# Performance work log

Measured on AMD Instinct MI355X. Metric: run time of the kernel, lower is better.

Reference implementation:

```python
import jax, jax.numpy as jnp
import numpy as np

T, B, D, H = 512, 64, 256, 512


def setup_inputs() -> dict:
    key = jax.random.key(0)
    k1, k2, k3, k4 = jax.random.split(key, 4)
    x = jax.random.normal(k1, (T, B, D), dtype=jnp.float32)
    should_reset = jax.random.randint(k2, (T, B), 0, 2, dtype=jnp.int32)
    # Linear([x, h]) -> 4H gates, Haiku/PyTorch-style fan-in init scale
    scale = 1.0 / np.sqrt(D + H)
    W = jax.random.normal(k3, (D + H, 4 * H), dtype=jnp.float32) * scale
    b = jax.random.normal(k4, (4 * H,), dtype=jnp.float32) * scale
    return {"x": x, "should_reset": should_reset, "W": W, "b": b}


def reference(x, should_reset, W, b):
    """ResetLSTM forward (reverse=False). x:[T,B,D], should_reset:[T,B] -> [T,B,H]."""
    h0 = jnp.zeros((x.shape[1], H), dtype=x.dtype)
    c0 = jnp.zeros((x.shape[1], H), dtype=x.dtype)
    reset = should_reset.astype(x.dtype)[..., None]  # [T,B,1]

    def step(carry, inp):
        h, c = carry
        xt, rt = inp
        keep = 1.0 - rt
        h = h * keep
        c = c * keep
        gates = jnp.concatenate([xt, h], axis=-1) @ W + b  # [B,4H]
        i, g, f, o = jnp.split(gates, 4, axis=-1)
        f = jax.nn.sigmoid(f + 1.0)  # Haiku forget bias +1
        i = jax.nn.sigmoid(i)
        g = jnp.tanh(g)
        o = jax.nn.sigmoid(o)
        new_c = f * c + i * g
        new_h = o * jnp.tanh(new_c)
        return (new_h, new_c), new_h

    _, outputs = jax.lax.scan(step, (h0, c0), (x, reset))
    return outputs  # [T,B,H]
```

## Files before the change

### kernel.cpp

```cpp
#include <hip/hip_runtime.h>

#define TSTEPS 512
#define BATCH  64
#define DIN    256
#define HID    512
#define NCH    8
#define VR     512
#define NRB    16
#define NUB    32
#define NWG    512
#define NTHR   256
#define HSST   264
#define GST    67

typedef __attribute__((ext_vector_type(8))) _Float16 f16x8;
typedef __attribute__((ext_vector_type(4))) _Float16 f16x4;
typedef __attribute__((ext_vector_type(4))) float f32x4;
typedef __attribute__((ext_vector_type(2))) float f32x2;

#define MFMA16(A,B,C) __builtin_amdgcn_mfma_f32_16x16x32_f16(A,B,C,0,0,0)
#define ALDU64(p) __hip_atomic_load(const_cast<unsigned long long*>(p), __ATOMIC_RELAXED, __HIP_MEMORY_SCOPE_AGENT)
#define ALDU32(p) __hip_atomic_load(const_cast<unsigned*>(p), __ATOMIC_RELAXED, __HIP_MEMORY_SCOPE_AGENT)
#define ASTU32(p,v) __hip_atomic_store((p), (v), __ATOMIC_RELAXED, __HIP_MEMORY_SCOPE_AGENT)

__device__ __forceinline__ float sigm(float x) { return 1.0f / (1.0f + __expf(-x)); }

__global__ void conv_x(const float* __restrict__ x, _Float16* __restrict__ xh, int n4) {
  int i = blockIdx.x * 256 + threadIdx.x;
  if (i >= n4) return;
  float4 v = reinterpret_cast<const float4*>(x)[i];
  f16x4 o;
  o[0] = (_Float16)v.x; o[1] = (_Float16)v.y; o[2] = (_Float16)v.z; o[3] = (_Float16)v.w;
  *reinterpret_cast<f16x4*>(xh + (size_t)i * 4) = o;
}

__global__ void w_prep(const float* __restrict__ W,
                       _Float16* __restrict__ WxT, _Float16* __restrict__ WhT) {
  int idx = blockIdx.x * 256 + threadIdx.x;
  if (idx < NUB * 64 * 256) {
    int k = idx & 255, cc = (idx >> 8) & 63, ub = idx >> 14;
    int unit = cc >> 2, g = cc & 3;
    int gcol = g * HID + ub * 16 + unit;
    WxT[idx] = (_Float16)W[k * 2048 + gcol];
  } else if (idx < NUB * 64 * 256 + NUB * 64 * 512) {
    int j = idx - NUB * 64 * 256;
    int k = j & 511, cc = (j >> 9) & 63, ub = j >> 15;
    int unit = cc >> 2, g = cc & 3;
    int gcol = g * HID + ub * 16 + unit;
    WhT[j] = (_Float16)W[(DIN + k) * 2048 + gcol];
  }
}

__global__ void seg_prep(const int* __restrict__ rst, int* __restrict__ tS,
                         int* __restrict__ segLen, int* __restrict__ maxLenB) {
  __shared__ int sMax[NRB];
  const int b = threadIdx.x;
  if (b < NRB) sMax[b] = 0;
  __syncthreads();
  int cut[NCH + 1];
  cut[0] = 0; cut[NCH] = TSTEPS;
  for (int c = 1; c < NCH; ++c) {
    int t = c * 64;
    while (t < TSTEPS && rst[t * BATCH + b] == 0) ++t;
    cut[c] = t;
  }
  for (int c = 1; c < NCH; ++c) if (cut[c] < cut[c - 1]) cut[c] = cut[c - 1];
  for (int c = 0; c < NCH; ++c) {
    int vr = c * 64 + b;
    tS[vr] = cut[c];
    int L = cut[c + 1] - cut[c];
    segLen[vr] = L;
    atomicMax(&sMax[c * 2 + (b >> 5)], L);
  }
  __syncthreads();
  if (b < NRB) maxLenB[b] = sMax[b];
}

__global__ void __launch_bounds__(NTHR, 2)
lstm_persistent(const _Float16* __restrict__ xh,
                const int* __restrict__ rst,
                const float* __restrict__ bias,
                float* __restrict__ out,
                unsigned long long* __restrict__ hb,
                unsigned* __restrict__ flags,
                const _Float16* __restrict__ WxT,
                const _Float16* __restrict__ WhT,
                const int* __restrict__ tS,
                const int* __restrict__ segLen,
                const int* __restrict__ maxLenB) {
  __shared__ _Float16 hS[32 * HSST];
  __shared__ float gateS[32 * GST];
  __shared__ float biasS[64];

  const int tid = threadIdx.x, wg = blockIdx.x;
  const int rb = wg >> 5, ub = wg & 31;
  const int vr0 = rb * 32;
  const int lane = tid & 63, wave = tid >> 6;
  const int colA = lane & 15, klo = (lane >> 4) * 8;

  f16x8 wx[8], wh[16];
  {
    const _Float16* px = WxT + ((size_t)ub * 64 + wave * 16 + colA) * 256 + klo;
    const _Float16* ph = WhT + ((size_t)ub * 64 + wave * 16 + colA) * 512 + klo;
#pragma unroll
    for (int ch = 0; ch < 8; ++ch) wx[ch] = *(const f16x8*)(px + ch * 32);
#pragma unroll
    for (int ch = 0; ch < 16; ++ch) wh[ch] = *(const f16x8*)(ph + ch * 32);
  }
  if (tid < 64) {
    int unit = tid >> 2, g = tid & 3;
    biasS[tid] = bias[g * HID + ub * 16 + unit];
  }

  int tSr0 = tS[vr0 + colA];
  int tSr1 = tS[vr0 + 16 + colA];

  const int crow = tid & 31, p = tid >> 5;
  const int vrc = vr0 + crow, bc = vrc & 63;
  const int tSc_ = tS[vrc], lenc_ = segLen[vrc];
  const int ML = maxLenB[rb];
  float cA = 0.f, cB = 0.f;

  __syncthreads();
  float bA[4], bB[4];
#pragma unroll
  for (int g = 0; g < 4; ++g) { bA[g] = biasS[8 * p + g]; bB[g] = biasS[8 * p + 4 + g]; }

  const int srow = tid >> 3, ss = tid & 7;

  for (int k = 0; k < ML; ++k) {
    f16x8 xq0[8], xq1[8];
    {
      int t0 = tSr0 + k; if (t0 > TSTEPS - 1) t0 = TSTEPS - 1;
      int t1 = tSr1 + k; if (t1 > TSTEPS - 1) t1 = TSTEPS - 1;
      const int b0 = (vr0 + colA) & 63, b1 = (vr0 + 16 + colA) & 63;
      const _Float16* x0 = xh + ((size_t)t0 * BATCH + b0) * DIN + klo;
      const _Float16* x1 = xh + ((size_t)t1 * BATCH + b1) * DIN + klo;
#pragma unroll
      for (int ch = 0; ch < 8; ++ch) {
        xq0[ch] = *(const f16x8*)(x0 + ch * 32);
        xq1[ch] = *(const f16x8*)(x1 + ch * 32);
      }
    }
    __builtin_amdgcn_sched_barrier(0);

    if (k) {
      if (tid < NUB) {
        const unsigned tgt = (unsigned)k;
        while (ALDU32(flags + (rb * NUB + tid) * 16) < tgt) __builtin_amdgcn_s_sleep(1);
      }
      __syncthreads();
      asm volatile("" ::: "memory");
    }

    f32x4 acc0 = {0.f, 0.f, 0.f, 0.f}, acc1 = {0.f, 0.f, 0.f, 0.f};

    if (k) {
      const size_t hbase = (size_t)(k & 1) * (VR * 128) + (size_t)(vr0 + srow) * 128;
      unsigned long long hq[8];
#pragma unroll
      for (int j = 0; j < 8; ++j) hq[j] = ALDU64(hb + hbase + ss + 8 * j);
      __builtin_amdgcn_sched_barrier(0);
#pragma unroll
      for (int ch = 0; ch < 8; ++ch) {
        acc0 = MFMA16(xq0[ch], wx[ch], acc0);
        acc1 = MFMA16(xq1[ch], wx[ch], acc1);
      }
#pragma unroll
      for (int j = 0; j < 8; ++j)
        *(unsigned long long*)&hS[srow * HSST + (ss + 8 * j) * 4] = hq[j];
      __syncthreads();
#pragma unroll
      for (int j = 0; j < 8; ++j) hq[j] = ALDU64(hb + hbase + 64 + ss + 8 * j);
      __builtin_amdgcn_sched_barrier(0);
#pragma unroll
      for (int ch = 0; ch < 8; ++ch) {
        f16x8 a0 = *(const f16x8*)&hS[colA * HSST + ch * 32 + klo];
        f16x8 a1 = *(const f16x8*)&hS[(16 + colA) * HSST + ch * 32 + klo];
        acc0 = MFMA16(a0, wh[ch], acc0);
        acc1 = MFMA16(a1, wh[ch], acc1);
      }
      __syncthreads();
#pragma unroll
      for (int j = 0; j < 8; ++j)
        *(unsigned long long*)&hS[srow * HSST + (ss + 8 * j) * 4] = hq[j];
      __syncthreads();
#pragma unroll
      for (int ch = 0; ch < 8; ++ch) {
        f16x8 a0 = *(const f16x8*)&hS[colA * HSST + ch * 32 + klo];
        f16x8 a1 = *(const f16x8*)&hS[(16 + colA) * HSST + ch * 32 + klo];
        acc0 = MFMA16(a0, wh[8 + ch], acc0);
        acc1 = MFMA16(a1, wh[8 + ch], acc1);
      }
    } else {
#pragma unroll
      for (int ch = 0; ch < 8; ++ch) {
        acc0 = MFMA16(xq0[ch], wx[ch], acc0);
        acc1 = MFMA16(xq1[ch], wx[ch], acc1);
      }
    }

#pragma unroll
    for (int rr = 0; rr < 4; ++rr) {
      int row0 = (lane >> 4) * 4 + rr;
      gateS[row0 * GST + wave * 16 + colA]        = acc0[rr];
      gateS[(16 + row0) * GST + wave * 16 + colA] = acc1[rr];
    }

    {
      int kidx = tSc_ + k + 1; if (kidx > TSTEPS - 1) kidx = TSTEPS - 1;
      float keep = 1.0f - (float)rst[kidx * BATCH + bc];
      const float* g = &gateS[crow * GST + 8 * p];
      float i0 = sigm(g[0] + bA[0]);
      float t0 = tanhf(g[1] + bA[1]);
      float f0 = sigm(g[2] + bA[2] + 1.0f);
      float o0 = sigm(g[3] + bA[3]);
      float i1 = sigm(g[4] + bB[0]);
      float t1 = tanhf(g[5] + bB[1]);
      float f1 = sigm(g[6] + bB[2] + 1.0f);
      float o1 = sigm(g[7] + bB[3]);
      float cn0 = f0 * cA + i0 * t0, cn1 = f1 * cB + i1 * t1;
      float hn0 = o0 * tanhf(cn0),   hn1 = o1 * tanhf(cn1);
      cA = cn0 * keep; cB = cn1 * keep;
      if (k < lenc_) {
        f32x2 o2 = {hn0, hn1};
        *(f32x2*)&out[((size_t)(tSc_ + k) * BATCH + bc) * HID + ub * 16 + 2 * p] = o2;
      }
      if (k + 1 < ML) {
        union { _Float16 f[2]; unsigned u; } cv;
        cv.f[0] = (_Float16)(hn0 * keep);
        cv.f[1] = (_Float16)(hn1 * keep);
        unsigned* hb32 = (unsigned*)(hb + (size_t)((k + 1) & 1) * (VR * 128) + (size_t)vrc * 128);
        ASTU32(hb32 + ub * 8 + p, cv.u);
      }
    }

    if (k + 1 < ML) {
      __syncthreads();
      if (tid == 0) ASTU32(flags + wg * 16, (unsigned)(k + 1));
    }
  }
}

extern "C" void kernel_launch(void* const* d_in, const int* in_sizes, int n_in,
                              void* d_out, int out_size, void* d_ws, size_t ws_size,
                              hipStream_t stream) {
  const float* x   = (const float*)d_in[0];
  const int*   rst = (const int*)d_in[1];
  const float* W   = (const float*)d_in[2];
  const float* b   = (const float*)d_in[3];
  float* out = (float*)d_out;
  char* ws = (char*)d_ws;

  unsigned*           flags  = (unsigned*)(ws + 0);
  int*                tSp    = (int*)(ws + 32768);
  int*                segLen = (int*)(ws + 34816);
  int*                maxLenB= (int*)(ws + 36864);
  unsigned long long* hb     = (unsigned long long*)(ws + 40960);
  _Float16*           xh     = (_Float16*)(ws + 40960 + 1048576);
  _Float16*           WxT    = (_Float16*)(ws + 40960 + 1048576 + 16777216);
  _Float16*           WhT    = (_Float16*)(ws + 40960 + 1048576 + 16777216 + 1048576);

  hipMemsetAsync(ws, 0, 32768, stream);

  int n4 = TSTEPS * BATCH * DIN / 4;
  hipLaunchKernelGGL(conv_x, dim3(n4 / 256), dim3(256), 0, stream, x, xh, n4);
  hipLaunchKernelGGL(w_prep, dim3(6144), dim3(256), 0, stream, W, WxT, WhT);
  hipLaunchKernelGGL(seg_prep, dim3(1), dim3(64), 0, stream, rst, tSp, segLen, maxLenB);

  hipLaunchKernelGGL(lstm_persistent, dim3(NWG), dim3(NTHR), 0, stream,
                     xh, rst, b, out, hb, flags, WxT, WhT, tSp, segLen, maxLenB);
}
```

Baseline: 563.5 us.

## Load full hidden state in one pass and move output store after flag publish

Widens the LDS hidden-state buffer so the whole 512-wide h row is staged at once. This replaces two half-loads and their extra barriers with a single pass of 16-byte cache-bypassing loads, followed by 16 MFMA steps. The x-projection MFMAs now run before the flag wait instead of being interleaved with the h loads. The global output store moves after the flag publish so it stays off the cross-workgroup critical path. The trade-offs are more LDS per workgroup, a barrier now taken on every step, and the loss of overlap between the h loads and the x MFMAs.

```diff
diff --git a/kernel.cpp b/kernel.cpp
--- a/kernel.cpp
+++ b/kernel.cpp
@@ -10,7 +10,7 @@
 #define NUB    32
 #define NWG    512
 #define NTHR   256
-#define HSST   264
+#define HSST   520
 #define GST    67
 
 typedef __attribute__((ext_vector_type(8))) _Float16 f16x8;
@@ -19,11 +19,14 @@
 typedef __attribute__((ext_vector_type(2))) float f32x2;
 
 #define MFMA16(A,B,C) __builtin_amdgcn_mfma_f32_16x16x32_f16(A,B,C,0,0,0)
-#define ALDU64(p) __hip_atomic_load(const_cast<unsigned long long*>(p), __ATOMIC_RELAXED, __HIP_MEMORY_SCOPE_AGENT)
 #define ALDU32(p) __hip_atomic_load(const_cast<unsigned*>(p), __ATOMIC_RELAXED, __HIP_MEMORY_SCOPE_AGENT)
 #define ASTU32(p,v) __hip_atomic_store((p), (v), __ATOMIC_RELAXED, __HIP_MEMORY_SCOPE_AGENT)
 
 __device__ __forceinline__ float sigm(float x) { return 1.0f / (1.0f + __expf(-x)); }
+
+__device__ __forceinline__ void gld16_cc(f16x8& d, const void* p) {
+  asm volatile("global_load_dwordx4 %0, %1, off sc0 sc1" : "=v"(d) : "v"(p));
+}
 
 __global__ void conv_x(const float* __restrict__ x, _Float16* __restrict__ xh, int n4) {
   int i = blockIdx.x * 256 + threadIdx.x;
@@ -129,7 +132,7 @@
   const int srow = tid >> 3, ss = tid & 7;
 
   for (int k = 0; k < ML; ++k) {
-    f16x8 xq0[8], xq1[8];
+    f32x4 acc0 = {0.f, 0.f, 0.f, 0.f}, acc1 = {0.f, 0.f, 0.f, 0.f};
     {
       int t0 = tSr0 + k; if (t0 > TSTEPS - 1) t0 = TSTEPS - 1;
       int t1 = tSr1 + k; if (t1 > TSTEPS - 1) t1 = TSTEPS - 1;
@@ -138,11 +141,12 @@
       const _Float16* x1 = xh + ((size_t)t1 * BATCH + b1) * DIN + klo;
 #pragma unroll
       for (int ch = 0; ch < 8; ++ch) {
-        xq0[ch] = *(const f16x8*)(x0 + ch * 32);
-        xq1[ch] = *(const f16x8*)(x1 + ch * 32);
-      }
-    }
-    __builtin_amdgcn_sched_barrier(0);
+        f16x8 a0 = *(const f16x8*)(x0 + ch * 32);
+        f16x8 a1 = *(const f16x8*)(x1 + ch * 32);
+        acc0 = MFMA16(a0, wx[ch], acc0);
+        acc1 = MFMA16(a1, wx[ch], acc1);
+      }
+    }
 
     if (k) {
       if (tid < NUB) {
@@ -151,53 +155,29 @@
       }
       __syncthreads();
       asm volatile("" ::: "memory");
-    }
-
-    f32x4 acc0 = {0.f, 0.f, 0.f, 0.f}, acc1 = {0.f, 0.f, 0.f, 0.f};
-
-    if (k) {
-      const size_t hbase = (size_t)(k & 1) * (VR * 128) + (size_t)(vr0 + srow) * 128;
-      unsigned long long hq[8];
-#pragma unroll
-      for (int j = 0; j < 8; ++j) hq[j] = ALDU64(hb + hbase + ss + 8 * j);
-      __builtin_amdgcn_sched_barrier(0);
-#pragma unroll
-      for (int ch = 0; ch < 8; ++ch) {
-        acc0 = MFMA16(xq0[ch], wx[ch], acc0);
-        acc1 = MFMA16(xq1[ch], wx[ch], acc1);
-      }
-#pragma unroll
-      for (int j = 0; j < 8; ++j)
-        *(unsigned long long*)&hS[srow * HSST + (ss + 8 * j) * 4] = hq[j];
+
+      {
+        const char* hbase = (const char*)hb
+            + (((size_t)(k & 1) * (VR * 128) + (size_t)(vr0 + srow) * 128) << 3)
+            + ss * 16;
+        f16x8 hq[8];
+#pragma unroll
+        for (int j = 0; j < 8; ++j) gld16_cc(hq[j], hbase + j * 128);
+        asm volatile("s_waitcnt vmcnt(0)" ::: "memory");
+        __builtin_amdgcn_sched_barrier(0);
+#pragma unroll
+        for (int j = 0; j < 8; ++j)
+          *(f16x8*)&hS[srow * HSST + ss * 8 + j * 64] = hq[j];
+      }
       __syncthreads();
-#pragma unroll
-      for (int j = 0; j < 8; ++j) hq[j] = ALDU64(hb + hbase + 64 + ss + 8 * j);
-      __builtin_amdgcn_sched_barrier(0);
-#pragma unroll
-      for (int ch = 0; ch < 8; ++ch) {
+
+#pragma unroll
+      for (int ch = 0; ch < 16; ++ch) {
         f16x8 a0 = *(const f16x8*)&hS[colA * HSST + ch * 32 + klo];
         f16x8 a1 = *(const f16x8*)&hS[(16 + colA) * HSST + ch * 32 + klo];
         acc0 = MFMA16(a0, wh[ch], acc0);
         acc1 = MFMA16(a1, wh[ch], acc1);
       }
-      __syncthreads();
-#pragma unroll
-      for (int j = 0; j < 8; ++j)
-        *(unsigned long long*)&hS[srow * HSST + (ss + 8 * j) * 4] = hq[j];
-      __syncthreads();
-#pragma unroll
-      for (int ch = 0; ch < 8; ++ch) {
-        f16x8 a0 = *(const f16x8*)&hS[colA * HSST + ch * 32 + klo];
-        f16x8 a1 = *(const f16x8*)&hS[(16 + colA) * HSST + ch * 32 + klo];
-        acc0 = MFMA16(a0, wh[8 + ch], acc0);
-        acc1 = MFMA16(a1, wh[8 + ch], acc1);
-      }
-    } else {
-#pragma unroll
-      for (int ch = 0; ch < 8; ++ch) {
-        acc0 = MFMA16(xq0[ch], wx[ch], acc0);
-        acc1 = MFMA16(xq1[ch], wx[ch], acc1);
-      }
     }
 
 #pragma unroll
@@ -207,6 +187,7 @@
       gateS[(16 + row0) * GST + wave * 16 + colA] = acc1[rr];
     }
 
+    float hn0, hn1;
     {
       int kidx = tSc_ + k + 1; if (kidx > TSTEPS - 1) kidx = TSTEPS - 1;
       float keep = 1.0f - (float)rst[kidx * BATCH + bc];
@@ -220,12 +201,8 @@
       float f1 = sigm(g[6] + bB[2] + 1.0f);
       float o1 = sigm(g[7] + bB[3]);
       float cn0 = f0 * cA + i0 * t0, cn1 = f1 * cB + i1 * t1;
-      float hn0 = o0 * tanhf(cn0),   hn1 = o1 * tanhf(cn1);
+      hn0 = o0 * tanhf(cn0); hn1 = o1 * tanhf(cn1);
       cA = cn0 * keep; cB = cn1 * keep;
-      if (k < lenc_) {
-        f32x2 o2 = {hn0, hn1};
-        *(f32x2*)&out[((size_t)(tSc_ + k) * BATCH + bc) * HID + ub * 16 + 2 * p] = o2;
-      }
       if (k + 1 < ML) {
         union { _Float16 f[2]; unsigned u; } cv;
         cv.f[0] = (_Float16)(hn0 * keep);
@@ -235,9 +212,12 @@
       }
     }
 
-    if (k + 1 < ML) {
-      __syncthreads();
-      if (tid == 0) ASTU32(flags + wg * 16, (unsigned)(k + 1));
+    __syncthreads();
+    if (k + 1 < ML && tid == 0) ASTU32(flags + wg * 16, (unsigned)(k + 1));
+
+    if (k < lenc_) {
+      f32x2 o2 = {hn0, hn1};
+      *(f32x2*)&out[((size_t)(tSc_ + k) * BATCH + bc) * HID + ub * 16 + 2 * p] = o2;
     }
   }
 }
```

Result: faster. 505.7 us (-10.3%).
